# Kernel tuning notes

Measured on AMD Instinct MI355X. Metric: run time of the kernel, lower is better.

## Reference

```python
import jax, jax.numpy as jnp
import numpy as np

# DeepSeek-V2 MLA dims (one tensor-parallel shard of 8)
H = 5120          # hidden size
S = 2048          # seq len
B = 1
NH = 16           # 128 heads / 8 devices
Q_LORA = 1536
KV_LORA = 512
NOPE = 128
ROPE = 64
QK = NOPE + ROPE  # 192 per-head q/k dim
VD = 128          # v head dim
DEVICE_NUM = 8
EPS = 1e-6


def rms_norm(x, w):
    v = jnp.mean(jnp.square(x.astype(jnp.float32)), axis=-1, keepdims=True)
    return (x * jax.lax.rsqrt(v + EPS)).astype(x.dtype) * w


def rope_cos_sin(position_ids, dim=ROPE, base=10000.0):
    inv_freq = 1.0 / (base ** (jnp.arange(0, dim, 2, dtype=jnp.float32) / dim))
    freqs = position_ids.astype(jnp.float32)[..., None] * inv_freq       # [B,S,dim/2]
    emb = jnp.concatenate([freqs, freqs], axis=-1)                        # [B,S,dim]
    return jnp.cos(emb), jnp.sin(emb)


def apply_rope(x, cos, sin):
    # DeepSeek interleaved reorder: view(b,h,s,d//2,2).transpose(-1,-2).reshape
    b, h, s, d = x.shape
    x = x.reshape(b, h, s, d // 2, 2).transpose(0, 1, 2, 4, 3).reshape(b, h, s, d)
    x1, x2 = x[..., : d // 2], x[..., d // 2:]
    rot = jnp.concatenate([-x2, x1], axis=-1)
    return x * cos[:, None] + rot * sin[:, None]


def setup_inputs() -> dict:
    key = jax.random.key(0)
    ks = jax.random.split(key, 8)
    sc = 0.02
    hidden_states = jax.random.normal(ks[0], (B, S, H), dtype=jnp.float32)
    position_ids = jnp.arange(S, dtype=jnp.int64 if jax.config.jax_enable_x64 else jnp.int32)[None, :].repeat(B, 0)
    attention_mask = jnp.triu(jnp.full((S, S), -1e9, dtype=jnp.float32), 1)[None, None]
    return {
        "hidden_states": hidden_states,
        "position_ids": position_ids,
        "attention_mask": attention_mask,
        "ln_w": jnp.ones((H,), jnp.float32),
        "q_a_w": jax.random.normal(ks[1], (Q_LORA, H), jnp.float32) * sc,
        "q_a_ln_w": jnp.ones((Q_LORA,), jnp.float32),
        "q_b_w": jax.random.normal(ks[2], (NH * QK, Q_LORA), jnp.float32) * sc,
        "kv_a_w": jax.random.normal(ks[3], (KV_LORA + ROPE, H), jnp.float32) * sc,
        "kv_a_ln_w": jnp.ones((KV_LORA,), jnp.float32),
        "kv_b_w": jax.random.normal(ks[4], (NH * (NOPE + VD), KV_LORA), jnp.float32) * sc,
        "o_w": jax.random.normal(ks[5], (H, NH * VD), jnp.float32) * sc,
    }


def reference(hidden_states, position_ids, attention_mask, ln_w, q_a_w, q_a_ln_w,
              q_b_w, kv_a_w, kv_a_ln_w, kv_b_w, o_w):
    b, s, _ = hidden_states.shape
    residual = hidden_states * (1.0 / DEVICE_NUM)
    x = rms_norm(hidden_states, ln_w)

    # Q path: low-rank down-proj + RMSNorm + up-proj
    q = rms_norm(x @ q_a_w.T, q_a_ln_w) @ q_b_w.T                # [b,s,NH*QK]
    q = q.reshape(b, s, NH, QK).transpose(0, 2, 1, 3)            # [b,NH,s,QK]
    q_nope, q_pe = q[..., :NOPE], q[..., NOPE:]

    # KV path: compressed latent + shared rope key
    ckv = x @ kv_a_w.T                                           # [b,s,KV_LORA+ROPE]
    c_kv, k_pe = ckv[..., :KV_LORA], ckv[..., KV_LORA:]
    k_pe = k_pe.reshape(b, s, 1, ROPE).transpose(0, 2, 1, 3)     # [b,1,s,ROPE]
    kv = rms_norm(c_kv, kv_a_ln_w) @ kv_b_w.T                    # [b,s,NH*(NOPE+VD)]
    kv = kv.reshape(b, s, NH, NOPE + VD).transpose(0, 2, 1, 3)
    k_nope, v = kv[..., :NOPE], kv[..., NOPE:]

    cos, sin = rope_cos_sin(position_ids)
    q_pe = apply_rope(q_pe, cos, sin)
    k_pe = apply_rope(k_pe, cos, sin)

    k = jnp.concatenate([k_nope, jnp.broadcast_to(k_pe, (b, NH, s, ROPE))], axis=-1)
    qf = jnp.concatenate([q_nope, q_pe], axis=-1)

    scores = jnp.einsum('bhqd,bhkd->bhqk', qf, k) * (1.0 / np.sqrt(QK))
    scores = scores + attention_mask
    probs = jax.nn.softmax(scores, axis=-1)
    attn = jnp.einsum('bhqk,bhkd->bhqd', probs, v)               # [b,NH,s,VD]

    out = attn.transpose(0, 2, 1, 3).reshape(b, s, NH * VD) @ o_w.T
    hidden = residual + out
    return hidden.astype(jnp.float32), k.astype(jnp.float32), v.astype(jnp.float32)
```

## Files before the change

kernel.cpp:

```cpp
#include <hip/hip_runtime.h>
#include <math.h>

typedef unsigned short u16;
typedef unsigned int u32;
typedef __attribute__((ext_vector_type(8))) short short8;
typedef __attribute__((ext_vector_type(4))) float f32x4;

#define NHEADS 16
static const int S      = 2048;
static const int Hd     = 5120;
static const int QLORA  = 1536;
static const int KVLORA = 512;
static const int NQK    = 192;
static const int NVD    = 128;
static const int QDIM   = 3072;
static const int KVDIM  = 4096;
static const int NFUSE  = 2176;

__device__ __forceinline__ u16 f2bf(float f) {
    union { float f; u32 u; } v; v.f = f;
    u32 r = v.u + 0x7FFFu + ((v.u >> 16) & 1u);
    return (u16)(r >> 16);
}
__device__ __forceinline__ float bf2f(u16 h) {
    union { u32 u; float f; } v; v.u = (u32)h << 16; return v.f;
}

__global__ void convert_all_kernel(const float* __restrict__ o_w,
                                   const float* __restrict__ q_a_w,
                                   const float* __restrict__ kv_a_w,
                                   const float* __restrict__ q_b_w,
                                   const float* __restrict__ kv_b_w,
                                   u16* __restrict__ o_wb, u16* __restrict__ Wf,
                                   u16* __restrict__ q_b_wb, u16* __restrict__ kv_b_wb) {
    long c = (long)blockIdx.x * 256 + threadIdx.x;
    const float* src; u16* dst; long nsrcc;
    if (c < 2621440L)      { src = o_w;    dst = o_wb;            nsrcc = 2621440L; }
    else if (c < 4587520L) { c -= 2621440L; src = q_a_w; dst = Wf; nsrcc = 1966080L; }
    else if (c < 5406720L) { c -= 4587520L; src = kv_a_w; dst = Wf + 7864320L; nsrcc = 737280L; }
    else if (c < 6586368L) { c -= 5406720L; src = q_b_w;  dst = q_b_wb;  nsrcc = 1179648L; }
    else if (c < 7110656L) { c -= 6586368L; src = kv_b_w; dst = kv_b_wb; nsrcc = 524288L; }
    else return;
    union { u16 h[4]; uint2 u; } p;
    if (c < nsrcc) {
        float4 v = *(const float4*)(src + c * 4);
        p.h[0] = f2bf(v.x); p.h[1] = f2bf(v.y); p.h[2] = f2bf(v.z); p.h[3] = f2bf(v.w);
    } else {
        p.h[0] = p.h[1] = p.h[2] = p.h[3] = 0;
    }
    *(uint2*)(dst + c * 4) = p.u;
}

__global__ void rmsnorm_bf16_kernel(const float* in, const float* __restrict__ w,
                                    u16* out, int D, int in_stride, int out_stride) {
    int row = blockIdx.x;
    const float* x = in + (size_t)row * in_stride;
    u16* y = out + (size_t)row * out_stride;
    float ss = 0.f;
    for (int i = threadIdx.x; i < D; i += blockDim.x) { float v = x[i]; ss += v * v; }
    #pragma unroll
    for (int off = 32; off > 0; off >>= 1) ss += __shfl_xor(ss, off);
    __shared__ float wsum[8];
    int wid = threadIdx.x >> 6, lane = threadIdx.x & 63;
    if (lane == 0) wsum[wid] = ss;
    __syncthreads();
    float tot = 0.f;
    int nw = blockDim.x >> 6;
    for (int i = 0; i < nw; ++i) tot += wsum[i];
    float scale = rsqrtf(tot / (float)D + 1e-6f);
    for (int i = threadIdx.x; i < D; i += blockDim.x) y[i] = f2bf(x[i] * scale * w[i]);
}

__global__ void rms_qkv_kernel(const u16* __restrict__ CF,
                               const float* __restrict__ qw, const float* __restrict__ kw,
                               u16* __restrict__ QAn, u16* __restrict__ CKVN) {
    const int row = blockIdx.x;
    const u16* x; u16* y; const float* w; int D;
    if (blockIdx.y == 0) {
        x = CF + (size_t)row * NFUSE;          y = QAn + (size_t)row * QLORA;
        w = qw; D = QLORA;
    } else {
        x = CF + (size_t)row * NFUSE + QLORA;  y = CKVN + (size_t)row * KVLORA;
        w = kw; D = KVLORA;
    }
    float ss = 0.f;
    for (int i = threadIdx.x; i < D; i += blockDim.x) { float v = bf2f(x[i]); ss += v * v; }
    #pragma unroll
    for (int off = 32; off > 0; off >>= 1) ss += __shfl_xor(ss, off);
    __shared__ float wsum[4];
    int wid = threadIdx.x >> 6, lane = threadIdx.x & 63;
    if (lane == 0) wsum[wid] = ss;
    __syncthreads();
    float tot = wsum[0] + wsum[1] + wsum[2] + wsum[3];
    float scale = rsqrtf(tot / (float)D + 1e-6f);
    for (int i = threadIdx.x; i < D; i += blockDim.x) y[i] = f2bf(bf2f(x[i]) * scale * w[i]);
}

template<int BM, bool SWZ, bool OBF>
__global__ __launch_bounds__(256) void gemm64_k(
    const u16* __restrict__ A, const u16* __restrict__ B, void* __restrict__ Cv,
    int M, int N, int K, const float* __restrict__ resid) {
    constexpr int MR = BM / 32;
    constexpr int ALOADS = (BM * 128) / 4096;
    __shared__ u16 As[2][BM * 64];
    __shared__ u16 Bs[2][128 * 64];

    int bm, bn;
    if constexpr (SWZ) {
        const int lin = blockIdx.x + blockIdx.y * gridDim.x;
        const int nwg = gridDim.x * gridDim.y;
        const int xcd = lin & 7, off = lin >> 3;
        const int q = nwg >> 3, r = nwg & 7;
        const int wg = (xcd < r ? xcd * (q + 1) : r * (q + 1) + (xcd - r) * q) + off;
        bm = (wg % gridDim.y) * BM;
        bn = (wg / gridDim.y) * 128;
    } else {
        bm = blockIdx.y * BM;
        bn = blockIdx.x * 128;
    }

    const int tid = threadIdx.x;
    const int w = tid >> 6, lane = tid & 63;
    const int wr = w >> 1, wc = w & 1;
    const int fr = lane & 15, kg = lane >> 4;
    const int swz = (fr & 7) << 4;

    f32x4 acc[MR][4];
    #pragma unroll
    for (int i = 0; i < MR; ++i)
        #pragma unroll
        for (int j = 0; j < 4; ++j) acc[i][j] = (f32x4){0.f, 0.f, 0.f, 0.f};

    const size_t K2 = (size_t)K * 2;

    auto STAGE = [&](int buf, int kt) {
        const char* ga = (const char*)A + ((size_t)bm * K + (size_t)kt * 64) * 2;
        const char* gb = (const char*)B + ((size_t)bn * K + (size_t)kt * 64) * 2;
        #pragma unroll
        for (int j = 0; j < ALOADS; ++j) {
            const int D = j * 4096 + tid * 16;
            const int r = D >> 7, c = (D & 127) ^ ((r & 7) << 4);
            __builtin_amdgcn_global_load_lds(
                (const __attribute__((address_space(1))) void*)(ga + (size_t)r * K2 + c),
                (__attribute__((address_space(3))) void*)((char*)&As[buf][0] + D), 16, 0, 0);
        }
        #pragma unroll
        for (int j = 0; j < 4; ++j) {
            const int D = j * 4096 + tid * 16;
            const int r = D >> 7, c = (D & 127) ^ ((r & 7) << 4);
            __builtin_amdgcn_global_load_lds(
                (const __attribute__((address_space(1))) void*)(gb + (size_t)r * K2 + c),
                (__attribute__((address_space(3))) void*)((char*)&Bs[buf][0] + D), 16, 0, 0);
        }
    };
    auto COMP = [&](int buf) {
        #pragma unroll
        for (int s = 0; s < 2; ++s) {
            short8 af[MR], bfr[4];
            #pragma unroll
            for (int i = 0; i < MR; ++i) {
                const int row = wr * (BM / 2) + i * 16 + fr;
                af[i] = *(const short8*)((const char*)&As[buf][0] +
                         row * 128 + ((s * 64 + kg * 16) ^ swz));
            }
            #pragma unroll
            for (int i = 0; i < 4; ++i) {
                const int row = wc * 64 + i * 16 + fr;
                bfr[i] = *(const short8*)((const char*)&Bs[buf][0] +
                          row * 128 + ((s * 64 + kg * 16) ^ swz));
            }
            #pragma unroll
            for (int mi = 0; mi < MR; ++mi)
                #pragma unroll
                for (int ni = 0; ni < 4; ++ni)
                    acc[mi][ni] = __builtin_amdgcn_mfma_f32_16x16x32_bf16(
                        af[mi], bfr[ni], acc[mi][ni], 0, 0, 0);
        }
    };

    const int nk = K >> 6;
    STAGE(0, 0);
    asm volatile("s_waitcnt vmcnt(0)" ::: "memory");
    __builtin_amdgcn_s_barrier();
    for (int kt = 0; kt < nk; ++kt) {
        if (kt + 1 < nk) STAGE((kt + 1) & 1, kt + 1);
        COMP(kt & 1);
        asm volatile("s_waitcnt vmcnt(0)" ::: "memory");
        __builtin_amdgcn_s_barrier();
    }

    #pragma unroll
    for (int mi = 0; mi < MR; ++mi)
        #pragma unroll
        for (int ni = 0; ni < 4; ++ni)
            #pragma unroll
            for (int r2 = 0; r2 < 4; ++r2) {
                int row = bm + wr * (BM / 2) + mi * 16 + kg * 4 + r2;
                int col = bn + wc * 64 + ni * 16 + fr;
                size_t idx = (size_t)row * N + col;
                float v = acc[mi][ni][r2];
                if constexpr (OBF) {
                    ((u16*)Cv)[idx] = f2bf(v);
                } else {
                    if (resid) v += resid[idx] * 0.125f;
                    ((float*)Cv)[idx] = v;
                }
            }
}

__global__ __launch_bounds__(256) void gemm_qkv_kernel(
    const u16* __restrict__ QAn, const u16* __restrict__ CKVN,
    const u16* __restrict__ q_b_wb, const u16* __restrict__ kv_b_wb,
    u16* __restrict__ Qbf, u16* __restrict__ KVb) {
    __shared__ u16 As[4][64 * 32];
    __shared__ u16 Bs[4][128 * 32];
    const bool isQ = blockIdx.x < 24;
    const u16* A = isQ ? QAn : CKVN;
    const u16* B = isQ ? q_b_wb : kv_b_wb;
    const int K = isQ ? QLORA : KVLORA;
    const int bn = (isQ ? blockIdx.x : blockIdx.x - 24) * 128;
    const int bm = blockIdx.y * 64;

    const int tid = threadIdx.x;
    const int w = tid >> 6, lane = tid & 63;
    const int wr = w >> 1, wc = w & 1;
    const int fr = lane & 15, kg = lane >> 4;

    f32x4 acc[2][4];
    #pragma unroll
    for (int i = 0; i < 2; ++i)
        #pragma unroll
        for (int j = 0; j < 4; ++j) acc[i][j] = (f32x4){0.f, 0.f, 0.f, 0.f};

    const int srow = lane >> 2;
    const int scol = (lane & 3) * 8;
    const u16* Ap0 = A + (size_t)(bm + w * 16 + srow) * K + scol;
    const u16* Bp0 = B + (size_t)(bn + w * 32 + srow) * K + scol;
    const u16* Bp1 = Bp0 + (size_t)16 * K;
    const int lda0 = (w * 16) * 32;
    const int ldb0 = (w * 32) * 32;
    const int ldb1 = (w * 32 + 16) * 32;

    auto STAGE = [&](int buf, int kk) {
        __builtin_amdgcn_global_load_lds(
            (const __attribute__((address_space(1))) void*)(Ap0 + kk),
            (__attribute__((address_space(3))) void*)&As[buf][lda0], 16, 0, 0);
        __builtin_amdgcn_global_load_lds(
            (const __attribute__((address_space(1))) void*)(Bp0 + kk),
            (__attribute__((address_space(3))) void*)&Bs[buf][ldb0], 16, 0, 0);
        __builtin_amdgcn_global_load_lds(
            (const __attribute__((address_space(1))) void*)(Bp1 + kk),
            (__attribute__((address_space(3))) void*)&Bs[buf][ldb1], 16, 0, 0);
    };
    auto COMP = [&](int buf) {
        short8 af[2], bfr[4];
        #pragma unroll
        for (int i = 0; i < 2; ++i)
            af[i] = *(const short8*)&As[buf][(wr * 32 + i * 16 + fr) * 32 + kg * 8];
        #pragma unroll
        for (int i = 0; i < 4; ++i)
            bfr[i] = *(const short8*)&Bs[buf][(wc * 64 + i * 16 + fr) * 32 + kg * 8];
        #pragma unroll
        for (int mi = 0; mi < 2; ++mi)
            #pragma unroll
            for (int ni = 0; ni < 4; ++ni)
                acc[mi][ni] = __builtin_amdgcn_mfma_f32_16x16x32_bf16(af[mi], bfr[ni],
                                                                      acc[mi][ni], 0, 0, 0);
    };

    const int nk = K >> 5;
    STAGE(0, 0);
    STAGE(1, 32);
    for (int kt = 0; kt < nk; ++kt) {
        if (kt + 2 < nk) {
            STAGE((kt + 2) & 3, (kt + 2) << 5);
            asm volatile("s_waitcnt vmcnt(6)" ::: "memory");
        } else if (kt + 1 < nk) {
            asm volatile("s_waitcnt vmcnt(3)" ::: "memory");
        } else {
            asm volatile("s_waitcnt vmcnt(0)" ::: "memory");
        }
        __builtin_amdgcn_s_barrier();
        COMP(kt & 3);
    }

    #pragma unroll
    for (int mi = 0; mi < 2; ++mi)
        #pragma unroll
        for (int ni = 0; ni < 4; ++ni)
            #pragma unroll
            for (int r2 = 0; r2 < 4; ++r2) {
                int row = bm + wr * 32 + mi * 16 + kg * 4 + r2;
                int col = bn + wc * 64 + ni * 16 + fr;
                float v = acc[mi][ni][r2];
                if (isQ) {
                    size_t idx = ((size_t)(col / 192) * S + row) * 192 + (col % 192);
                    Qbf[idx] = f2bf(v);
                } else {
                    KVb[(size_t)row * KVDIM + col] = f2bf(v);
                }
            }
}

__global__ void rope_q_inplace_kernel(u16* __restrict__ Qbf, const int* __restrict__ pos) {
    const int s = blockIdx.x;
    const int t = threadIdx.x;
    const int hh = t >> 5, j = t & 31;
    float ps = (float)pos[s];
    float inv_freq = 1.0f / powf(10000.0f, (float)j * (1.0f / 32.0f));
    float ang = ps * inv_freq;
    float c = cosf(ang), sn = sinf(ang);
    u16* base = Qbf + ((size_t)hh * S + s) * NQK;
    float a = bf2f(base[128 + 2 * j]), b = bf2f(base[128 + 2 * j + 1]);
    __syncthreads();
    base[128 + j] = f2bf(a * c - b * sn);
    base[160 + j] = f2bf(b * c + a * sn);
}

__global__ __launch_bounds__(256) void build_kv64_kernel(
    const u16* __restrict__ KVb, const u16* __restrict__ CF,
    const int* __restrict__ pos_ids,
    float* __restrict__ Kout, float* __restrict__ Vout,
    u16* __restrict__ Kbf, u16* __restrict__ Vtb) {
    const int s0 = blockIdx.x * 64;
    const int h  = blockIdx.y;
    const int t  = threadIdx.x;
    __shared__ u16 T[64][132];

    #pragma unroll
    for (int it = 0; it < 4; ++it) {
        int i = t + it * 256;
        int row = i >> 4, c8 = (i & 15) * 8;
        int s = s0 + row;
        union { uint4 u; u16 hx[8]; } v;
        v.u = *(const uint4*)(KVb + (size_t)s * KVDIM + h * 256 + c8);
        size_t kidx = ((size_t)h * S + s) * NQK + c8;
        *(uint4*)(Kbf + kidx) = v.u;
        float4 f0 = {bf2f(v.hx[0]), bf2f(v.hx[1]), bf2f(v.hx[2]), bf2f(v.hx[3])};
        float4 f1 = {bf2f(v.hx[4]), bf2f(v.hx[5]), bf2f(v.hx[6]), bf2f(v.hx[7])};
        *(float4*)(Kout + kidx) = f0;
        *(float4*)(Kout + kidx + 4) = f1;
    }
    #pragma unroll
    for (int it = 0; it < 4; ++it) {
        int i = t + it * 256;
        int row = i >> 4, c8 = (i & 15) * 8;
        int s = s0 + row;
        union { uint4 u; uint2 d[2]; u16 hx[8]; } v;
        v.u = *(const uint4*)(KVb + (size_t)s * KVDIM + h * 256 + 128 + c8);
        *(uint2*)&T[row][c8]     = v.d[0];
        *(uint2*)&T[row][c8 + 4] = v.d[1];
        size_t vidx = ((size_t)h * S + s) * NVD + c8;
        float4 f0 = {bf2f(v.hx[0]), bf2f(v.hx[1]), bf2f(v.hx[2]), bf2f(v.hx[3])};
        float4 f1 = {bf2f(v.hx[4]), bf2f(v.hx[5]), bf2f(v.hx[6]), bf2f(v.hx[7])};
        *(float4*)(Vout + vidx) = f0;
        *(float4*)(Vout + vidx + 4) = f1;
    }
    #pragma unroll
    for (int it = 0; it < 8; ++it) {
        int i = t + it * 256;
        int row = i >> 5, j = i & 31;
        int s = s0 + row;
        float ps = (float)pos_ids[s];
        float inv_freq = 1.0f / powf(10000.0f, (float)j * (1.0f / 32.0f));
        float ang = ps * inv_freq;
        float c = cosf(ang), sn = sinf(ang);
        u32 pr = *(const u32*)(CF + (size_t)s * NFUSE + QLORA + KVLORA + 2 * j);
        float a = bf2f((u16)pr), b = bf2f((u16)(pr >> 16));
        float k0 = a * c - b * sn;
        float k1 = b * c + a * sn;
        size_t kidx = ((size_t)h * S + s) * NQK;
        Kout[kidx + 128 + j] = k0;
        Kout[kidx + 160 + j] = k1;
        Kbf[kidx + 128 + j] = f2bf(k0);
        Kbf[kidx + 160 + j] = f2bf(k1);
    }
    __syncthreads();
    const int d = t >> 1, half = t & 1;
    #pragma unroll
    for (int c = 0; c < 4; ++c) {
        u16 tmp[8];
        #pragma unroll
        for (int e = 0; e < 8; ++e) tmp[e] = T[half * 32 + c * 8 + e][d];
        *(uint4*)(Vtb + ((size_t)h * NVD + d) * S + s0 + half * 32 + c * 8) = *(uint4*)tmp;
    }
}

__global__ __launch_bounds__(256) void attn_mfma_kernel(
    const u16* __restrict__ Qbf, const u16* __restrict__ Kb,
    const u16* __restrict__ Vtb, u16* __restrict__ ATb) {
    const int h = blockIdx.y;
    const int q0 = (gridDim.x - 1 - blockIdx.x) * 64;
    const int tid = threadIdx.x;
    const int w = tid >> 6, lane = tid & 63;
    const int fr = lane & 15, kg = lane >> 4;

    __shared__ __align__(16) u16 Ks[2][64 * 192];
    __shared__ __align__(16) u16 Vts[2][128 * 64];

    int kSrc[6], vSrc[4];
    #pragma unroll
    for (int i = 0; i < 6; ++i) {
        int D = (w * 6 + i) * 1024 + lane * 16;
        int row = D / 384, wb = D - row * 384;
        kSrc[i] = row * 384 + (wb ^ ((row & 7) << 4));
    }
    #pragma unroll
    for (int i = 0; i < 4; ++i) {
        int D = (w * 4 + i) * 1024 + lane * 16;
        int row = D >> 7, wb = D & 127;
        vSrc[i] = row * (S * 2) + (wb ^ ((row & 7) << 4));
    }
    const char* Kg = (const char*)(Kb + (size_t)h * S * NQK);
    const char* Vg = (const char*)(Vtb + (size_t)h * NVD * S);

    auto STAGE = [&](int buf, int kt) {
        const size_t krow = (size_t)kt * 64;
        #pragma unroll
        for (int i = 0; i < 6; ++i)
            __builtin_amdgcn_global_load_lds(
                (const __attribute__((address_space(1))) void*)(Kg + krow * 384 + kSrc[i]),
                (__attribute__((address_space(3))) void*)((char*)&Ks[buf][0] + (w * 6 + i) * 1024), 16, 0, 0);
        #pragma unroll
        for (int i = 0; i < 4; ++i)
            __builtin_amdgcn_global_load_lds(
                (const __attribute__((address_space(1))) void*)(Vg + krow * 2 + vSrc[i]),
                (__attribute__((address_space(3))) void*)((char*)&Vts[buf][0] + (w * 4 + i) * 1024), 16, 0, 0);
    };

    short8 qf[6];
    {
        const u16* qrow = Qbf + ((size_t)h * S + q0 + w * 16 + fr) * NQK;
        #pragma unroll
        for (int kb = 0; kb < 6; ++kb)
            qf[kb] = *(const short8*)(qrow + kb * 32 + kg * 8);
    }

    f32x4 o[8];
    #pragma unroll
    for (int ni = 0; ni < 8; ++ni) o[ni] = (f32x4){0.f, 0.f, 0.f, 0.f};
    float mrow = -1e30f, lrow = 0.f;
    const float scale = 0.0721687836487032f;
    const int qg = q0 + w * 16 + fr;
    const int swz = (fr & 7) << 4;
    const int nt = (q0 >> 6) + 1;

    STAGE(0, 0);
    asm volatile("s_waitcnt vmcnt(0)" ::: "memory");
    __builtin_amdgcn_s_barrier();

    for (int t = 0; t < nt; ++t) {
        if (t + 1 < nt) STAGE((t + 1) & 1, t + 1);
        const int buf = t & 1;
        const int k0 = t * 64;

        f32x4 sacc[4];
        #pragma unroll
        for (int mi = 0; mi < 4; ++mi) sacc[mi] = (f32x4){0.f, 0.f, 0.f, 0.f};
        __builtin_amdgcn_s_setprio(1);
        #pragma unroll
        for (int mi = 0; mi < 4; ++mi)
            #pragma unroll
            for (int kb = 0; kb < 6; ++kb) {
                const short8 kf = *(const short8*)((const char*)&Ks[buf][0] +
                    (mi * 16 + fr) * 384 + ((kb * 64 + kg * 16) ^ swz));
                sacc[mi] = __builtin_amdgcn_mfma_f32_16x16x32_bf16(kf, qf[kb], sacc[mi], 0, 0, 0);
            }
        __builtin_amdgcn_s_setprio(0);

        const bool diag = (k0 == q0);
        float p[4][4];
        float mx = -1e30f;
        #pragma unroll
        for (int mi = 0; mi < 4; ++mi)
            #pragma unroll
            for (int r = 0; r < 4; ++r) {
                float v = sacc[mi][r] * scale;
                if (diag && (k0 + mi * 16 + kg * 4 + r > qg)) v = -1e30f;
                p[mi][r] = v;
                mx = fmaxf(mx, v);
            }
        mx = fmaxf(mx, __shfl_xor(mx, 16));
        mx = fmaxf(mx, __shfl_xor(mx, 32));
        float mnew = fmaxf(mrow, mx);
        float corr = __expf(mrow - mnew);
        float psum = 0.f;
        #pragma unroll
        for (int mi = 0; mi < 4; ++mi)
            #pragma unroll
            for (int r = 0; r < 4; ++r) {
                float e = __expf(p[mi][r] - mnew);
                p[mi][r] = e;
                psum += e;
            }
        psum += __shfl_xor(psum, 16);
        psum += __shfl_xor(psum, 32);
        lrow = lrow * corr + psum;
        mrow = mnew;
        float corr_r[4];
        #pragma unroll
        for (int r = 0; r < 4; ++r) corr_r[r] = __shfl(corr, kg * 4 + r);
        #pragma unroll
        for (int ni = 0; ni < 8; ++ni) {
            o[ni][0] *= corr_r[0]; o[ni][1] *= corr_r[1];
            o[ni][2] *= corr_r[2]; o[ni][3] *= corr_r[3];
        }

        u32 pk0[4], pk1[4];
        #pragma unroll
        for (int mi = 0; mi < 4; ++mi) {
            pk0[mi] = (u32)f2bf(p[mi][0]) | ((u32)f2bf(p[mi][1]) << 16);
            pk1[mi] = (u32)f2bf(p[mi][2]) | ((u32)f2bf(p[mi][3]) << 16);
        }
        const int srcA = 2 * (kg & 1) * 16 + fr;
        const int srcB = srcA + 16;
        const int hsel = kg >> 1;
        short8 pa[2];
        #pragma unroll
        for (int ks = 0; ks < 2; ++ks) {
            u32 a0 = (u32)__shfl((int)pk0[ks * 2], srcA), b0 = (u32)__shfl((int)pk0[ks * 2 + 1], srcA);
            u32 a1 = (u32)__shfl((int)pk1[ks * 2], srcA), b1 = (u32)__shfl((int)pk1[ks * 2 + 1], srcA);
            u32 a2 = (u32)__shfl((int)pk0[ks * 2], srcB), b2 = (u32)__shfl((int)pk0[ks * 2 + 1], srcB);
            u32 a3 = (u32)__shfl((int)pk1[ks * 2], srcB), b3 = (u32)__shfl((int)pk1[ks * 2 + 1], srcB);
            union { u32 u[4]; short8 s8; } cvt;
            cvt.u[0] = hsel ? b0 : a0;
            cvt.u[1] = hsel ? b1 : a1;
            cvt.u[2] = hsel ? b2 : a2;
            cvt.u[3] = hsel ? b3 : a3;
            pa[ks] = cvt.s8;
        }

        __builtin_amdgcn_s_setprio(1);
        #pragma unroll
        for (int ks = 0; ks < 2; ++ks)
            #pragma unroll
            for (int ni = 0; ni < 8; ++ni) {
                const short8 vf = *(const short8*)((const char*)&Vts[buf][0] +
                    (ni * 16 + fr) * 128 + ((ks * 64 + kg * 16) ^ swz));
                o[ni] = __builtin_amdgcn_mfma_f32_16x16x32_bf16(pa[ks], vf, o[ni], 0, 0, 0);
            }
        __builtin_amdgcn_s_setprio(0);

        asm volatile("s_waitcnt vmcnt(0)" ::: "memory");
        __builtin_amdgcn_s_barrier();
    }

    float inv = 1.f / lrow;
    float inv_r[4];
    #pragma unroll
    for (int r = 0; r < 4; ++r) inv_r[r] = __shfl(inv, kg * 4 + r);
    u16* outp = ATb + (size_t)(q0 + w * 16 + kg * 4) * (NHEADS * NVD) + h * NVD + fr;
    #pragma unroll
    for (int ni = 0; ni < 8; ++ni)
        #pragma unroll
        for (int r = 0; r < 4; ++r)
            outp[(size_t)r * (NHEADS * NVD) + ni * 16] = f2bf(o[ni][r] * inv_r[r]);
}

extern "C" void kernel_launch(void* const* d_in, const int* in_sizes, int n_in,
                              void* d_out, int out_size, void* d_ws, size_t ws_size,
                              hipStream_t stream) {
    (void)in_sizes; (void)n_in; (void)out_size; (void)ws_size;
    const float* hidden    = (const float*)d_in[0];
    const int*   pos       = (const int*)d_in[1];
    const float* ln_w      = (const float*)d_in[3];
    const float* q_a_w     = (const float*)d_in[4];
    const float* q_a_ln_w  = (const float*)d_in[5];
    const float* q_b_w     = (const float*)d_in[6];
    const float* kv_a_w    = (const float*)d_in[7];
    const float* kv_a_ln_w = (const float*)d_in[8];
    const float* kv_b_w    = (const float*)d_in[9];
    const float* o_w       = (const float*)d_in[10];

    float* OUT_H = (float*)d_out;
    float* OUT_K = OUT_H + (size_t)S * Hd;
    float* OUT_V = OUT_K + (size_t)NHEADS * S * NQK;

    char* ws = (char*)d_ws;
    u16*   o_wb    = (u16*)(ws);
    u16*   Wf      = (u16*)(ws + 20971520);
    u16*   Qbf     = (u16*)(ws + 20971520);
    u16*   Vtb     = (u16*)(ws + 33554432);
    u16*   Xb      = (u16*)(ws + 43253760);
    u16*   Kbf     = (u16*)(ws + 43253760);
    u16*   ATb     = (u16*)(ws + 55836672);
    u16*   CF      = (u16*)(ws + 64225280);
    u16*   QAn     = (u16*)(ws + 73138176);
    u16*   CKVN    = (u16*)(ws + 79429632);
    u16*   q_b_wb  = (u16*)(ws + 81526784);
    u16*   kv_b_wb = (u16*)(ws + 90963968);
    u16*   KVb     = (u16*)(ws + 95158272);

    convert_all_kernel<<<27776, 256, 0, stream>>>(o_w, q_a_w, kv_a_w, q_b_w, kv_b_w,
                                                  o_wb, Wf, q_b_wb, kv_b_wb);
    rmsnorm_bf16_kernel<<<S, 256, 0, stream>>>(hidden, ln_w, Xb, Hd, Hd, Hd);
    gemm64_k<128, true, true><<<dim3(NFUSE / 128, S / 128), 256, 0, stream>>>(Xb, Wf, CF, S, NFUSE, Hd, nullptr);
    rms_qkv_kernel<<<dim3(S, 2), 256, 0, stream>>>(CF, q_a_ln_w, kv_a_ln_w, QAn, CKVN);
    gemm_qkv_kernel<<<dim3(56, S / 64), 256, 0, stream>>>(QAn, CKVN, q_b_wb, kv_b_wb, Qbf, KVb);
    rope_q_inplace_kernel<<<S, 512, 0, stream>>>(Qbf, pos);
    build_kv64_kernel<<<dim3(S / 64, NHEADS), 256, 0, stream>>>(KVb, CF, pos, OUT_K, OUT_V, Kbf, Vtb);
    attn_mfma_kernel<<<dim3(S / 64, NHEADS), 256, 0, stream>>>(Qbf, Kbf, Vtb, ATb);
    gemm64_k<64, false, false><<<dim3(Hd / 128, S / 64), 256, 0, stream>>>(ATb, o_wb, OUT_H, S, Hd, NHEADS * NVD, hidden);
}
```

Baseline: 386.6 us.

## Use 64-wide swizzled K tiles in QKV GEMM and skip softmax rescaling

```diff
diff --git a/kernel.cpp b/kernel.cpp
--- a/kernel.cpp
+++ b/kernel.cpp
@@ -208,12 +208,12 @@
             }
 }
 
-__global__ __launch_bounds__(256) void gemm_qkv_kernel(
+__global__ __launch_bounds__(256) void gemm_qkv64_kernel(
     const u16* __restrict__ QAn, const u16* __restrict__ CKVN,
     const u16* __restrict__ q_b_wb, const u16* __restrict__ kv_b_wb,
     u16* __restrict__ Qbf, u16* __restrict__ KVb) {
-    __shared__ u16 As[4][64 * 32];
-    __shared__ u16 Bs[4][128 * 32];
+    __shared__ u16 As[2][64 * 64];
+    __shared__ u16 Bs[2][128 * 64];
     const bool isQ = blockIdx.x < 24;
     const u16* A = isQ ? QAn : CKVN;
     const u16* B = isQ ? q_b_wb : kv_b_wb;
@@ -225,6 +225,7 @@
     const int w = tid >> 6, lane = tid & 63;
     const int wr = w >> 1, wc = w & 1;
     const int fr = lane & 15, kg = lane >> 4;
+    const int swz = (fr & 7) << 4;
 
     f32x4 acc[2][4];
     #pragma unroll
@@ -232,56 +233,62 @@
         #pragma unroll
         for (int j = 0; j < 4; ++j) acc[i][j] = (f32x4){0.f, 0.f, 0.f, 0.f};
 
-    const int srow = lane >> 2;
-    const int scol = (lane & 3) * 8;
-    const u16* Ap0 = A + (size_t)(bm + w * 16 + srow) * K + scol;
-    const u16* Bp0 = B + (size_t)(bn + w * 32 + srow) * K + scol;
-    const u16* Bp1 = Bp0 + (size_t)16 * K;
-    const int lda0 = (w * 16) * 32;
-    const int ldb0 = (w * 32) * 32;
-    const int ldb1 = (w * 32 + 16) * 32;
-
-    auto STAGE = [&](int buf, int kk) {
-        __builtin_amdgcn_global_load_lds(
-            (const __attribute__((address_space(1))) void*)(Ap0 + kk),
-            (__attribute__((address_space(3))) void*)&As[buf][lda0], 16, 0, 0);
-        __builtin_amdgcn_global_load_lds(
-            (const __attribute__((address_space(1))) void*)(Bp0 + kk),
-            (__attribute__((address_space(3))) void*)&Bs[buf][ldb0], 16, 0, 0);
-        __builtin_amdgcn_global_load_lds(
-            (const __attribute__((address_space(1))) void*)(Bp1 + kk),
-            (__attribute__((address_space(3))) void*)&Bs[buf][ldb1], 16, 0, 0);
+    const size_t K2 = (size_t)K * 2;
+
+    auto STAGE = [&](int buf, int kt) {
+        const char* ga = (const char*)A + ((size_t)bm * K + (size_t)kt * 64) * 2;
+        const char* gb = (const char*)B + ((size_t)bn * K + (size_t)kt * 64) * 2;
+        #pragma unroll
+        for (int j = 0; j < 2; ++j) {
+            const int D = j * 4096 + tid * 16;
+            const int r = D >> 7, c = (D & 127) ^ ((r & 7) << 4);
+            __builtin_amdgcn_global_load_lds(
+                (const __attribute__((address_space(1))) void*)(ga + (size_t)r * K2 + c),
+                (__attribute__((address_space(3))) void*)((char*)&As[buf][0] + D), 16, 0, 0);
+        }
+        #pragma unroll
+        for (int j = 0; j < 4; ++j) {
+            const int D = j * 4096 + tid * 16;
+            const int r = D >> 7, c = (D & 127) ^ ((r & 7) << 4);
+            __builtin_amdgcn_global_load_lds(
+                (const __attribute__((address_space(1))) void*)(gb + (size_t)r * K2 + c),
+                (__attribute__((address_space(3))) void*)((char*)&Bs[buf][0] + D), 16, 0, 0);
+        }
     };
     auto COMP = [&](int buf) {
-        short8 af[2], bfr[4];
-        #pragma unroll
-        for (int i = 0; i < 2; ++i)
-            af[i] = *(const short8*)&As[buf][(wr * 32 + i * 16 + fr) * 32 + kg * 8];
-        #pragma unroll
-        for (int i = 0; i < 4; ++i)
-            bfr[i] = *(const short8*)&Bs[buf][(wc * 64 + i * 16 + fr) * 32 + kg * 8];
-        #pragma unroll
-        for (int mi = 0; mi < 2; ++mi)
-            #pragma unroll
-            for (int ni = 0; ni < 4; ++ni)
-                acc[mi][ni] = __builtin_amdgcn_mfma_f32_16x16x32_bf16(af[mi], bfr[ni],
-                                                                      acc[mi][ni], 0, 0, 0);
+        #pragma unroll
+        for (int s = 0; s < 2; ++s) {
+            short8 af[2], bfr[4];
+            #pragma unroll
+            for (int i = 0; i < 2; ++i) {
+                const int row = wr * 32 + i * 16 + fr;
+                af[i] = *(const short8*)((const char*)&As[buf][0] +
+                         row * 128 + ((s * 64 + kg * 16) ^ swz));
+            }
+            #pragma unroll
+            for (int i = 0; i < 4; ++i) {
+                const int row = wc * 64 + i * 16 + fr;
+                bfr[i] = *(const short8*)((const char*)&Bs[buf][0] +
+                          row * 128 + ((s * 64 + kg * 16) ^ swz));
+            }
+            #pragma unroll
+            for (int mi = 0; mi < 2; ++mi)
+                #pragma unroll
+                for (int ni = 0; ni < 4; ++ni)
+                    acc[mi][ni] = __builtin_amdgcn_mfma_f32_16x16x32_bf16(
+                        af[mi], bfr[ni], acc[mi][ni], 0, 0, 0);
+        }
     };
 
-    const int nk = K >> 5;
+    const int nk = K >> 6;
     STAGE(0, 0);
-    STAGE(1, 32);
+    asm volatile("s_waitcnt vmcnt(0)" ::: "memory");
+    __builtin_amdgcn_s_barrier();
     for (int kt = 0; kt < nk; ++kt) {
-        if (kt + 2 < nk) {
-            STAGE((kt + 2) & 3, (kt + 2) << 5);
-            asm volatile("s_waitcnt vmcnt(6)" ::: "memory");
-        } else if (kt + 1 < nk) {
-            asm volatile("s_waitcnt vmcnt(3)" ::: "memory");
-        } else {
-            asm volatile("s_waitcnt vmcnt(0)" ::: "memory");
-        }
+        if (kt + 1 < nk) STAGE((kt + 1) & 1, kt + 1);
+        COMP(kt & 1);
+        asm volatile("s_waitcnt vmcnt(0)" ::: "memory");
         __builtin_amdgcn_s_barrier();
-        COMP(kt & 3);
     }
 
     #pragma unroll
@@ -482,8 +489,8 @@
             }
         mx = fmaxf(mx, __shfl_xor(mx, 16));
         mx = fmaxf(mx, __shfl_xor(mx, 32));
-        float mnew = fmaxf(mrow, mx);
-        float corr = __expf(mrow - mnew);
+        const bool noresc = __all(mx <= mrow + 8.0f);
+        float mnew = noresc ? mrow : fmaxf(mrow, mx);
         float psum = 0.f;
         #pragma unroll
         for (int mi = 0; mi < 4; ++mi)
@@ -495,15 +502,20 @@
             }
         psum += __shfl_xor(psum, 16);
         psum += __shfl_xor(psum, 32);
-        lrow = lrow * corr + psum;
-        mrow = mnew;
-        float corr_r[4];
-        #pragma unroll
-        for (int r = 0; r < 4; ++r) corr_r[r] = __shfl(corr, kg * 4 + r);
-        #pragma unroll
-        for (int ni = 0; ni < 8; ++ni) {
-            o[ni][0] *= corr_r[0]; o[ni][1] *= corr_r[1];
-            o[ni][2] *= corr_r[2]; o[ni][3] *= corr_r[3];
+        if (noresc) {
+            lrow += psum;
+        } else {
+            float corr = __expf(mrow - mnew);
+            lrow = lrow * corr + psum;
+            mrow = mnew;
+            float corr_r[4];
+            #pragma unroll
+            for (int r = 0; r < 4; ++r) corr_r[r] = __shfl(corr, kg * 4 + r);
+            #pragma unroll
+            for (int ni = 0; ni < 8; ++ni) {
+                o[ni][0] *= corr_r[0]; o[ni][1] *= corr_r[1];
+                o[ni][2] *= corr_r[2]; o[ni][3] *= corr_r[3];
+            }
         }
 
         u32 pk0[4], pk1[4];
@@ -596,7 +608,7 @@
     rmsnorm_bf16_kernel<<<S, 256, 0, stream>>>(hidden, ln_w, Xb, Hd, Hd, Hd);
     gemm64_k<128, true, true><<<dim3(NFUSE / 128, S / 128), 256, 0, stream>>>(Xb, Wf, CF, S, NFUSE, Hd, nullptr);
     rms_qkv_kernel<<<dim3(S, 2), 256, 0, stream>>>(CF, q_a_ln_w, kv_a_ln_w, QAn, CKVN);
-    gemm_qkv_kernel<<<dim3(56, S / 64), 256, 0, stream>>>(QAn, CKVN, q_b_wb, kv_b_wb, Qbf, KVb);
+    gemm_qkv64_kernel<<<dim3(56, S / 64), 256, 0, stream>>>(QAn, CKVN, q_b_wb, kv_b_wb, Qbf, KVb);
     rope_q_inplace_kernel<<<S, 512, 0, stream>>>(Qbf, pos);
     build_kv64_kernel<<<dim3(S / 64, NHEADS), 256, 0, stream>>>(KVb, CF, pos, OUT_K, OUT_V, Kbf, Vtb);
     attn_mfma_kernel<<<dim3(S / 64, NHEADS), 256, 0, stream>>>(Qbf, Kbf, Vtb, ATb);
```

New measurement: 376.7 us. 2.5% less time.
